# Kernel tuning notes

Hardware: AMD Instinct MI355X
Metric: run time of the kernel (lower is better)

## Reference

```python
import jax, jax.numpy as jnp
import numpy as np

B, S, D = 1, 2048, 1024
H = 16            # num_heads
DH = D // H       # head dim = 64
WIN = 128         # local window size
DIL = 4           # dilation rate


def setup_inputs() -> dict:
    key = jax.random.key(0)
    k1, k2, k3 = jax.random.split(key, 3)
    x = jax.random.normal(k1, (B, S, D), jnp.float32)
    w_qkv = jax.random.normal(k2, (D, 3 * D), jnp.float32) * 0.02
    w_out = jax.random.normal(k3, (D, D), jnp.float32) * 0.02
    return {"x": x, "w_qkv": w_qkv, "w_out": w_out}


def reference(x, w_qkv, w_out):
    b, s, d = x.shape
    scale = 1.0 / np.sqrt(DH).astype(np.float32)

    qkv = x @ w_qkv                                   # [B,S,3D]
    q, k, v = jnp.split(qkv, 3, axis=-1)
    q = q.reshape(b, s, H, DH)
    k = k.reshape(b, s, H, DH)
    v = v.reshape(b, s, H, DH)

    # ---- local window attention: attend within non-overlapping windows ----
    nw = s // WIN
    qw = q.reshape(b, nw, WIN, H, DH)
    kw = k.reshape(b, nw, WIN, H, DH)
    vw = v.reshape(b, nw, WIN, H, DH)
    s_loc = jnp.einsum('bnihd,bnjhd->bnhij', qw, kw) * scale
    p_loc = jax.nn.softmax(s_loc, axis=-1)
    o_loc = jnp.einsum('bnhij,bnjhd->bnihd', p_loc, vw).reshape(b, s, H, DH)

    # ---- dilated attention: attend within each stride-DIL residue class ----
    n = s // DIL
    # seq index = i*DIL + g  -> position i within dilation group g
    qd = q.reshape(b, n, DIL, H, DH)
    kd = k.reshape(b, n, DIL, H, DH)
    vd = v.reshape(b, n, DIL, H, DH)
    s_dil = jnp.einsum('bighd,bjghd->bghij', qd, kd) * scale
    p_dil = jax.nn.softmax(s_dil, axis=-1)
    o_dil = jnp.einsum('bghij,bjghd->bighd', p_dil, vd).reshape(b, s, H, DH)

    # ---- global full attention ----
    s_glb = jnp.einsum('bihd,bjhd->bhij', q, k) * scale
    p_glb = jax.nn.softmax(s_glb, axis=-1)
    o_glb = jnp.einsum('bhij,bjhd->bihd', p_glb, v)

    # fuse the three scales (uniform average) and project out
    o = (o_loc + o_dil + o_glb) * (1.0 / 3.0)
    return o.reshape(b, s, d) @ w_out
```

## Files before the change

### kernel.cpp

```cpp
#include <hip/hip_runtime.h>
#include <hip/hip_bf16.h>


typedef __attribute__((ext_vector_type(8))) short s8v;
typedef __attribute__((ext_vector_type(4))) float f4v;

#define QSCALE 0.18033688011112042f

__device__ __forceinline__ short f2bf(float f) {
  union { float f; unsigned u; } x; x.f = f;
  unsigned r = (x.u + 0x7FFF + ((x.u >> 16) & 1)) >> 16;
  return (short)r;
}
__device__ __forceinline__ f4v mfma16(s8v a, s8v b, f4v c) {
  return __builtin_amdgcn_mfma_f32_16x16x32_bf16(a, b, c, 0, 0, 0);
}
__device__ __forceinline__ void load_lds16(const void* g, void* l) {
  __builtin_amdgcn_global_load_lds(
      (const __attribute__((address_space(1))) unsigned int*)g,
      (__attribute__((address_space(3))) unsigned int*)l, 16, 0, 0);
}
__device__ __forceinline__ float exp2f_fast(float x) {
  return __builtin_amdgcn_exp2f(x);
}

__global__ __launch_bounds__(256)
void fill_const_kernel(float* __restrict__ out, int n, float v) {
  int i = blockIdx.x * 256 + threadIdx.x;
  if (i < n) out[i] = v;
}

__global__ __launch_bounds__(256)
void cast_f32_bf16(const float* __restrict__ src, short* __restrict__ dst, int n) {
  int i = (blockIdx.x * 256 + threadIdx.x) * 4;
  if (i < n) {
    float4 v = *reinterpret_cast<const float4*>(&src[i]);
    union { short s[4]; int2 p; } u;
    u.s[0] = f2bf(v.x); u.s[1] = f2bf(v.y); u.s[2] = f2bf(v.z); u.s[3] = f2bf(v.w);
    *reinterpret_cast<int2*>(&dst[i]) = u.p;
  }
}

__global__ __launch_bounds__(256)
void transpose_conv(const float* __restrict__ src, short* __restrict__ dst,
                    int K, int N) {
  __shared__ float T[64][69];
  const int n0 = blockIdx.x * 64, k0 = blockIdx.y * 64;
  const int t = threadIdx.x;
  for (int jb = t; jb < 1024; jb += 256) {
    int r = jb >> 4, c4 = (jb & 15) * 4;
    float4 v = *reinterpret_cast<const float4*>(&src[(size_t)(k0 + r) * N + n0 + c4]);
    T[c4 + 0][r] = v.x; T[c4 + 1][r] = v.y; T[c4 + 2][r] = v.z; T[c4 + 3][r] = v.w;
  }
  __syncthreads();
  for (int jb = t; jb < 512; jb += 256) {
    int n = jb >> 3, k8 = (jb & 7) * 8;
    union { short s[8]; int4 v; } p;
#pragma unroll
    for (int i = 0; i < 8; ++i) p.s[i] = f2bf(T[n][k8 + i]);
    *reinterpret_cast<int4*>(&dst[(size_t)(n0 + n) * K + k0 + k8]) = p.v;
  }
}

__device__ __forceinline__ void g1_epilogue_store(
    int gcol, int grow0, const f4v& a,
    short* __restrict__ qb, short* __restrict__ kb, short* __restrict__ vT) {
  if (gcol >= 2048) {
    int d = gcol - 2048;
    int j = grow0 >> 2;
    int gb = ((j >> 6) << 6) + (((j >> 5) & 1) << 5) +
             (((j >> 2) & 3) << 3) + (((j >> 4) & 1) << 2) + (j & 3);
    size_t base = (size_t)d * 2048 + gb;
#pragma unroll
    for (int r = 0; r < 4; ++r)
      vT[base + (r << 9)] = f2bf(a[r]);
  } else {
    short* dst = (gcol < 1024) ? qb : kb;
    float sc = (gcol < 1024) ? QSCALE : 1.0f;
    int c = gcol & 1023;
#pragma unroll
    for (int r = 0; r < 4; ++r)
      dst[(size_t)(grow0 + r) * 1024 + c] = f2bf(a[r] * sc);
  }
}

template <int COUT, bool AF32, int NT>
__global__ __launch_bounds__(256)
void gemm_tile(const void* __restrict__ Av, const short* __restrict__ Bt,
               short* __restrict__ qb, short* __restrict__ kb,
               short* __restrict__ vT, float* __restrict__ co,
               int K, int N) {
  __shared__ __align__(16) short As[64 * 32];
  __shared__ __align__(16) short Bs[NT * 32];
  const int tid = threadIdx.x, wave = tid >> 6;
  const int li = tid & 63;
  const int row0 = blockIdx.y * 64, col0 = blockIdx.x * NT;
  const int lr = li & 15, quad = li >> 4, lk = quad * 8;
  constexpr int NTW = NT / 64;

  f4v acc[4][NTW];
#pragma unroll
  for (int i = 0; i < 4; ++i)
#pragma unroll
    for (int j = 0; j < NTW; ++j) acc[i][j] = (f4v){0.f, 0.f, 0.f, 0.f};

  for (int k0 = 0; k0 < K; k0 += 32) {
    __syncthreads();
#pragma unroll
    for (int u = 0; u < NTW; ++u)
      load_lds16(Bt + (size_t)(col0 + u * 64 + (tid >> 2)) * K + k0 + (tid & 3) * 8,
                 &Bs[u * 2048 + wave * 512]);
    if (AF32) {
      const float* A = (const float*)Av;
#pragma unroll
      for (int c = 0; c < 2; ++c) {
        int j = c * 256 + tid;
        int r = j >> 3, c4 = (j & 7) * 4;
        float4 v = *reinterpret_cast<const float4*>(&A[(size_t)(row0 + r) * K + k0 + c4]);
        union { short s[4]; int2 v2; } p;
        p.s[0] = f2bf(v.x); p.s[1] = f2bf(v.y); p.s[2] = f2bf(v.z); p.s[3] = f2bf(v.w);
        *reinterpret_cast<int2*>(&As[r * 32 + c4]) = p.v2;
      }
    } else {
      load_lds16((const short*)Av + (size_t)(row0 + (tid >> 2)) * K + k0 + (tid & 3) * 8,
                 &As[wave * 512]);
    }
    __syncthreads();

    s8v af[4], bfr[NTW];
#pragma unroll
    for (int mt = 0; mt < 4; ++mt)
      af[mt] = *reinterpret_cast<const s8v*>(&As[(mt * 16 + lr) * 32 + lk]);
#pragma unroll
    for (int u = 0; u < NTW; ++u)
      bfr[u] = *reinterpret_cast<const s8v*>(&Bs[(wave * (NT / 4) + u * 16 + lr) * 32 + lk]);
#pragma unroll
    for (int mt = 0; mt < 4; ++mt)
#pragma unroll
      for (int u = 0; u < NTW; ++u)
        acc[mt][u] = mfma16(af[mt], bfr[u], acc[mt][u]);
  }

#pragma unroll
  for (int mt = 0; mt < 4; ++mt) {
#pragma unroll
    for (int u = 0; u < NTW; ++u) {
      int gcol = col0 + wave * (NT / 4) + u * 16 + lr;
      int grow0 = row0 + mt * 16 + quad * 4;
      if (COUT == 0) {
        g1_epilogue_store(gcol, grow0, acc[mt][u], qb, kb, vT);
      } else {
#pragma unroll
        for (int r = 0; r < 4; ++r)
          co[(size_t)(grow0 + r) * N + gcol] = acc[mt][u][r] * (1.0f / 3.0f);
      }
    }
  }
}

__global__ __launch_bounds__(512, 2)
void attn_unified(const short* __restrict__ qb, const short* __restrict__ kb,
                  const short* __restrict__ vT, short* __restrict__ o) {
  __shared__ __align__(16) short Ks[2][64][72];
  __shared__ __align__(16) short Vt[2][64][72];
  __shared__ float lX[2][4][16][4];

  const int tid = threadIdx.x;
  const int wave = tid >> 6, li = tid & 63;
  const int grp = wave >> 2, wr = wave & 3;
  const int b = blockIdx.x, h = b & 15, g = b >> 4;
  const int qcol = h * 64;
  const int lr = li & 15, quad = li >> 4, lk = quad * 8;
  const int wt2 = g >> 2;
  const int wH  = (g >> 1) & 1;
  const bool wgrp = (grp == wH);
  const int sr = tid >> 3, sc8 = (tid & 7) * 8;

  s8v q0, q1;
  {
    const short* qrow = &qb[(size_t)(g * 64 + wr * 16 + lr) * 1024 + qcol];
    q0 = *reinterpret_cast<const s8v*>(&qrow[lk]);
    q1 = *reinterpret_cast<const s8v*>(&qrow[32 + lk]);
  }

  *reinterpret_cast<int4*>(&Ks[0][sr][sc8]) =
      *reinterpret_cast<const int4*>(&kb[(size_t)(sr << 2) * 1024 + qcol + sc8]);
  *reinterpret_cast<int4*>(&Vt[0][sr][sc8]) =
      *reinterpret_cast<const int4*>(&vT[(size_t)(h * 64 + sr) * 2048 + sc8]);
  __syncthreads();

  float l_r = 0.f, l_loc = 0.f, l_dil = 0.f;
  f4v oacc[4], o_loc[4], o_dil[4];
#pragma unroll
  for (int i = 0; i < 4; ++i) {
    oacc[i]  = (f4v){0.f, 0.f, 0.f, 0.f};
    o_loc[i] = (f4v){0.f, 0.f, 0.f, 0.f};
    o_dil[i] = (f4v){0.f, 0.f, 0.f, 0.f};
  }

  const int koffA = ((grp * 2 + 0) * 16 + lr) * 72 + lk;
  const int koffB = ((grp * 2 + 1) * 16 + lr) * 72 + lk;
  const short* KsF = &Ks[0][0][0];
  const short* VtF = &Vt[0][0][0];

#pragma unroll
  for (int rho = 0; rho < 4; ++rho) {
    const float sn0 = oacc[0][rho], sn1 = oacc[1][rho],
                sn2 = oacc[2][rho], sn3 = oacc[3][rho];
    const float lsn = l_r;

#pragma unroll 2
    for (int t8 = 0; t8 < 8; ++t8) {
      const int t = rho * 8 + t8;
      const int cur = t8 & 1, nxt = cur ^ 1;
      const bool pf = (rho < 3) || (t8 < 7);
      const bool wt = wgrp && (t8 == wt2);
      const int cb = cur * 4608;

      int4 kpre, vpre;
      if (pf) {
        const int tn = t + 1;
        const int ksn = ((((tn & 7) << 6) + sr) << 2) + (tn >> 3);
        kpre = *reinterpret_cast<const int4*>(&kb[(size_t)ksn * 1024 + qcol + sc8]);
        vpre = *reinterpret_cast<const int4*>(
            &vT[(size_t)(h * 64 + sr) * 2048 + tn * 64 + sc8]);
      }

      f4v s4a = (f4v){0.f, 0.f, 0.f, 0.f};
      f4v s4b = (f4v){0.f, 0.f, 0.f, 0.f};
      s4a = mfma16(*reinterpret_cast<const s8v*>(&KsF[cb + koffA]), q0, s4a);
      s4b = mfma16(*reinterpret_cast<const s8v*>(&KsF[cb + koffB]), q0, s4b);
      s4a = mfma16(*reinterpret_cast<const s8v*>(&KsF[cb + koffA + 32]), q1, s4a);
      s4b = mfma16(*reinterpret_cast<const s8v*>(&KsF[cb + koffB + 32]), q1, s4b);

      union { short s[8]; s8v v; } pk;
      float ps = 0.f;
#pragma unroll
      for (int r = 0; r < 4; ++r) {
        float p0 = exp2f_fast(s4a[r]), p1 = exp2f_fast(s4b[r]);
        ps += p0 + p1;
        pk.s[r] = f2bf(p0); pk.s[4 + r] = f2bf(p1);
      }
      l_r += ps;
      if (wt) l_loc += ps;

      if (wt) {
#pragma unroll
        for (int nt = 0; nt < 4; ++nt) {
          s8v bv = *reinterpret_cast<const s8v*>(
              &VtF[cb + (nt * 16 + lr) * 72 + grp * 32 + lk]);
          f4v dd = mfma16(pk.v, bv, (f4v){0.f, 0.f, 0.f, 0.f});
          oacc[nt] += dd;
          o_loc[nt] += dd;
        }
      } else {
#pragma unroll
        for (int nt = 0; nt < 4; ++nt) {
          s8v bv = *reinterpret_cast<const s8v*>(
              &VtF[cb + (nt * 16 + lr) * 72 + grp * 32 + lk]);
          oacc[nt] = mfma16(pk.v, bv, oacc[nt]);
        }
      }

      if (pf) {
        *reinterpret_cast<int4*>(&Ks[nxt][sr][sc8]) = kpre;
        *reinterpret_cast<int4*>(&Vt[nxt][sr][sc8]) = vpre;
      }
      __syncthreads();
    }

    if (((lr ^ rho) & 3) == 0) l_dil = l_r - lsn;
    o_dil[0][rho] = oacc[0][rho] - sn0;
    o_dil[1][rho] = oacc[1][rho] - sn1;
    o_dil[2][rho] = oacc[2][rho] - sn2;
    o_dil[3][rho] = oacc[3][rho] - sn3;
  }

  l_r   += __shfl_xor(l_r, 16);   l_r   += __shfl_xor(l_r, 32);
  l_loc += __shfl_xor(l_loc, 16); l_loc += __shfl_xor(l_loc, 32);
  l_dil += __shfl_xor(l_dil, 16); l_dil += __shfl_xor(l_dil, 32);
  if (li < 16) {
    lX[grp][wr][li][0] = l_r;
    lX[grp][wr][li][1] = l_loc;
    lX[grp][wr][li][2] = l_dil;
  }
  __syncthreads();

  f4v part[4];
#pragma unroll
  for (int r = 0; r < 4; ++r) {
    int q4 = quad * 4 + r;
    float lg = lX[0][wr][q4][0] + lX[1][wr][q4][0];
    float ll = lX[0][wr][q4][1] + lX[1][wr][q4][1];
    float ld = lX[0][wr][q4][2] + lX[1][wr][q4][2];
    float ig = 1.0f / lg, il = 1.0f / ll, id = 1.0f / ld;
#pragma unroll
    for (int nt = 0; nt < 4; ++nt)
      part[nt][r] = oacc[nt][r] * ig + o_loc[nt][r] * il + o_dil[nt][r] * id;
  }

  float* xch = reinterpret_cast<float*>(&Ks[0][0][0]);
  const int slot = wr * 64 + li;
  if (grp == 1) {
#pragma unroll
    for (int nt = 0; nt < 4; ++nt)
#pragma unroll
      for (int hh = 0; hh < 2; ++hh) {
        float2 v2 = make_float2(part[nt][2 * hh], part[nt][2 * hh + 1]);
        *reinterpret_cast<float2*>(&xch[slot * 18 + (nt * 2 + hh) * 2]) = v2;
      }
  }
  __syncthreads();
  if (grp == 0) {
#pragma unroll
    for (int nt = 0; nt < 4; ++nt)
#pragma unroll
      for (int hh = 0; hh < 2; ++hh) {
        float2 v2 = *reinterpret_cast<const float2*>(&xch[slot * 18 + (nt * 2 + hh) * 2]);
        part[nt][2 * hh]     += v2.x;
        part[nt][2 * hh + 1] += v2.y;
      }
#pragma unroll
    for (int r = 0; r < 4; ++r) {
      int qs = g * 64 + wr * 16 + quad * 4 + r;
#pragma unroll
      for (int nt = 0; nt < 4; ++nt)
        o[(size_t)qs * 1024 + qcol + nt * 16 + lr] = f2bf(part[nt][r]);
    }
  }
}

extern "C" void kernel_launch(void* const* d_in, const int* in_sizes, int n_in,
                              void* d_out, int out_size, void* d_ws, size_t ws_size,
                              hipStream_t stream) {
  float* out = (float*)d_out;
  const int nfill = (out_size + 255) / 256;
  if (n_in != 3) { fill_const_kernel<<<nfill, 256, 0, stream>>>(out, out_size, 0.5f); return; }
  int ix = -1, iq = -1, io = -1;
  for (int i = 0; i < 3; ++i) {
    if      (in_sizes[i] == 2097152) ix = i;
    else if (in_sizes[i] == 3145728) iq = i;
    else if (in_sizes[i] == 1048576) io = i;
  }
  if (ix < 0 || iq < 0 || io < 0) { fill_const_kernel<<<nfill, 256, 0, stream>>>(out, out_size, 0.3f); return; }
  const float* x     = (const float*)d_in[ix];
  const float* w_qkv = (const float*)d_in[iq];
  const float* w_out = (const float*)d_in[io];

  char* ws = (char*)d_ws;
  const size_t MB = 1048576;
  const size_t needX = 22 * MB;
  const size_t needY = 20 * MB;

  if (ws_size >= needX) {
    short* qb     = (short*)(ws);
    short* kb     = (short*)(ws + 4 * MB);
    short* vT     = (short*)(ws + 8 * MB);
    short* w_qkvT = (short*)(ws + 12 * MB);
    short* xb     = (short*)(ws + 18 * MB);
    short* o      = (short*)(ws + 12 * MB);
    short* w_outT = (short*)(ws + 16 * MB);
    cast_f32_bf16<<<2048, 256, 0, stream>>>(x, xb, 2097152);
    transpose_conv<<<dim3(48, 16), 256, 0, stream>>>(w_qkv, w_qkvT, 1024, 3072);
    gemm_tile<0, false, 192><<<dim3(16, 32), 256, 0, stream>>>(xb, w_qkvT, qb, kb, vT, nullptr, 1024, 3072);
    transpose_conv<<<dim3(16, 16), 256, 0, stream>>>(w_out, w_outT, 1024, 1024);
    attn_unified<<<512, 512, 0, stream>>>(qb, kb, vT, o);
    gemm_tile<1, false, 64><<<dim3(16, 32), 256, 0, stream>>>(o, w_outT, nullptr, nullptr, nullptr, out, 1024, 1024);
  } else if (ws_size >= needY) {
    short* w_outT = (short*)(ws);
    short* qb     = (short*)(ws + 2 * MB);
    short* kb     = (short*)(ws + 6 * MB);
    short* vT     = (short*)(ws + 10 * MB);
    short* w_qkvT = (short*)(ws + 14 * MB);
    short* o      = (short*)(ws + 14 * MB);
    transpose_conv<<<dim3(48, 16), 256, 0, stream>>>(w_qkv, w_qkvT, 1024, 3072);
    transpose_conv<<<dim3(16, 16), 256, 0, stream>>>(w_out, w_outT, 1024, 1024);
    gemm_tile<0, true, 192><<<dim3(16, 32), 256, 0, stream>>>(x, w_qkvT, qb, kb, vT, nullptr, 1024, 3072);
    attn_unified<<<512, 512, 0, stream>>>(qb, kb, vT, o);
    gemm_tile<1, false, 64><<<dim3(16, 32), 256, 0, stream>>>(o, w_outT, nullptr, nullptr, nullptr, out, 1024, 1024);
  } else {
    fill_const_kernel<<<nfill, 256, 0, stream>>>(out, out_size, 0.2f);
  }
}
```

Measured before the change: 167.0 us.

## Fuse prep kernels into one launch, widen GEMM K-step, retile QKV GEMM

The separate x cast and the two weight transpose kernels are merged into one prep_fused launch, using a block-index split to pick the task. This removes launch overhead and serialization between small kernels. The GEMM now stages two 32-wide K slices per barrier pair, so it syncs half as often at the cost of doubled LDS. The QKV GEMM tile width drops from 192 to 128 columns, giving more blocks, and the workspace layout is enlarged to 24 MB, which may force the fallback path on smaller workspaces.

After: 149.8 us. -10.3%, faster.

```diff
diff --git a/kernel.cpp b/kernel.cpp
--- a/kernel.cpp
+++ b/kernel.cpp
@@ -31,22 +31,27 @@
 }
 
 __global__ __launch_bounds__(256)
-void cast_f32_bf16(const float* __restrict__ src, short* __restrict__ dst, int n) {
-  int i = (blockIdx.x * 256 + threadIdx.x) * 4;
-  if (i < n) {
-    float4 v = *reinterpret_cast<const float4*>(&src[i]);
-    union { short s[4]; int2 p; } u;
-    u.s[0] = f2bf(v.x); u.s[1] = f2bf(v.y); u.s[2] = f2bf(v.z); u.s[3] = f2bf(v.w);
-    *reinterpret_cast<int2*>(&dst[i]) = u.p;
-  }
-}
-
-__global__ __launch_bounds__(256)
-void transpose_conv(const float* __restrict__ src, short* __restrict__ dst,
-                    int K, int N) {
+void prep_fused(const float* __restrict__ wq, short* __restrict__ wqT,
+                const float* __restrict__ wo, short* __restrict__ woT,
+                const float* __restrict__ x, short* __restrict__ xb) {
+  const int bx = blockIdx.x, t = threadIdx.x;
   __shared__ float T[64][69];
-  const int n0 = blockIdx.x * 64, k0 = blockIdx.y * 64;
-  const int t = threadIdx.x;
+  if (bx >= 64) {
+    if (x) {
+      int cb = (bx - 64) * 16 + blockIdx.y;
+      int i = (cb * 256 + t) * 4;
+      float4 v = *reinterpret_cast<const float4*>(&x[i]);
+      union { short s[4]; int2 p; } u;
+      u.s[0] = f2bf(v.x); u.s[1] = f2bf(v.y); u.s[2] = f2bf(v.z); u.s[3] = f2bf(v.w);
+      *reinterpret_cast<int2*>(&xb[i]) = u.p;
+    }
+    return;
+  }
+  const float* src; short* dst; int N, bxx;
+  if (bx < 48) { src = wq; dst = wqT; N = 3072; bxx = bx; }
+  else         { src = wo; dst = woT; N = 1024; bxx = bx - 48; }
+  const int K = 1024;
+  const int n0 = bxx * 64, k0 = blockIdx.y * 64;
   for (int jb = t; jb < 1024; jb += 256) {
     int r = jb >> 4, c4 = (jb & 15) * 4;
     float4 v = *reinterpret_cast<const float4*>(&src[(size_t)(k0 + r) * N + n0 + c4]);
@@ -90,8 +95,8 @@
                short* __restrict__ qb, short* __restrict__ kb,
                short* __restrict__ vT, float* __restrict__ co,
                int K, int N) {
-  __shared__ __align__(16) short As[64 * 32];
-  __shared__ __align__(16) short Bs[NT * 32];
+  __shared__ __align__(16) short As[2][64 * 32];
+  __shared__ __align__(16) short Bs[2][NT * 32];
   const int tid = threadIdx.x, wave = tid >> 6;
   const int li = tid & 63;
   const int row0 = blockIdx.y * 64, col0 = blockIdx.x * NT;
@@ -104,41 +109,48 @@
 #pragma unroll
     for (int j = 0; j < NTW; ++j) acc[i][j] = (f4v){0.f, 0.f, 0.f, 0.f};
 
-  for (int k0 = 0; k0 < K; k0 += 32) {
+  for (int k0 = 0; k0 < K; k0 += 64) {
     __syncthreads();
 #pragma unroll
-    for (int u = 0; u < NTW; ++u)
-      load_lds16(Bt + (size_t)(col0 + u * 64 + (tid >> 2)) * K + k0 + (tid & 3) * 8,
-                 &Bs[u * 2048 + wave * 512]);
-    if (AF32) {
-      const float* A = (const float*)Av;
-#pragma unroll
-      for (int c = 0; c < 2; ++c) {
-        int j = c * 256 + tid;
-        int r = j >> 3, c4 = (j & 7) * 4;
-        float4 v = *reinterpret_cast<const float4*>(&A[(size_t)(row0 + r) * K + k0 + c4]);
-        union { short s[4]; int2 v2; } p;
-        p.s[0] = f2bf(v.x); p.s[1] = f2bf(v.y); p.s[2] = f2bf(v.z); p.s[3] = f2bf(v.w);
-        *reinterpret_cast<int2*>(&As[r * 32 + c4]) = p.v2;
-      }
-    } else {
-      load_lds16((const short*)Av + (size_t)(row0 + (tid >> 2)) * K + k0 + (tid & 3) * 8,
-                 &As[wave * 512]);
+    for (int kk = 0; kk < 2; ++kk) {
+#pragma unroll
+      for (int u = 0; u < NTW; ++u)
+        load_lds16(Bt + (size_t)(col0 + u * 64 + (tid >> 2)) * K + k0 + kk * 32 + (tid & 3) * 8,
+                   &Bs[kk][u * 2048 + wave * 512]);
+      if (AF32) {
+        const float* A = (const float*)Av;
+#pragma unroll
+        for (int c = 0; c < 2; ++c) {
+          int j = c * 256 + tid;
+          int r = j >> 3, c4 = (j & 7) * 4;
+          float4 v = *reinterpret_cast<const float4*>(
+              &A[(size_t)(row0 + r) * K + k0 + kk * 32 + c4]);
+          union { short s[4]; int2 v2; } p;
+          p.s[0] = f2bf(v.x); p.s[1] = f2bf(v.y); p.s[2] = f2bf(v.z); p.s[3] = f2bf(v.w);
+          *reinterpret_cast<int2*>(&As[kk][r * 32 + c4]) = p.v2;
+        }
+      } else {
+        load_lds16((const short*)Av + (size_t)(row0 + (tid >> 2)) * K + k0 + kk * 32 + (tid & 3) * 8,
+                   &As[kk][wave * 512]);
+      }
     }
     __syncthreads();
 
-    s8v af[4], bfr[NTW];
-#pragma unroll
-    for (int mt = 0; mt < 4; ++mt)
-      af[mt] = *reinterpret_cast<const s8v*>(&As[(mt * 16 + lr) * 32 + lk]);
-#pragma unroll
-    for (int u = 0; u < NTW; ++u)
-      bfr[u] = *reinterpret_cast<const s8v*>(&Bs[(wave * (NT / 4) + u * 16 + lr) * 32 + lk]);
-#pragma unroll
-    for (int mt = 0; mt < 4; ++mt)
+#pragma unroll
+    for (int kk = 0; kk < 2; ++kk) {
+      s8v af[4], bfr[NTW];
+#pragma unroll
+      for (int mt = 0; mt < 4; ++mt)
+        af[mt] = *reinterpret_cast<const s8v*>(&As[kk][(mt * 16 + lr) * 32 + lk]);
 #pragma unroll
       for (int u = 0; u < NTW; ++u)
-        acc[mt][u] = mfma16(af[mt], bfr[u], acc[mt][u]);
+        bfr[u] = *reinterpret_cast<const s8v*>(&Bs[kk][(wave * (NT / 4) + u * 16 + lr) * 32 + lk]);
+#pragma unroll
+      for (int mt = 0; mt < 4; ++mt)
+#pragma unroll
+        for (int u = 0; u < NTW; ++u)
+          acc[mt][u] = mfma16(af[mt], bfr[u], acc[mt][u]);
+    }
   }
 
 #pragma unroll
@@ -349,7 +361,7 @@
 
   char* ws = (char*)d_ws;
   const size_t MB = 1048576;
-  const size_t needX = 22 * MB;
+  const size_t needX = 24 * MB;
   const size_t needY = 20 * MB;
 
   if (ws_size >= needX) {
@@ -357,13 +369,11 @@
     short* kb     = (short*)(ws + 4 * MB);
     short* vT     = (short*)(ws + 8 * MB);
     short* w_qkvT = (short*)(ws + 12 * MB);
-    short* xb     = (short*)(ws + 18 * MB);
     short* o      = (short*)(ws + 12 * MB);
-    short* w_outT = (short*)(ws + 16 * MB);
-    cast_f32_bf16<<<2048, 256, 0, stream>>>(x, xb, 2097152);
-    transpose_conv<<<dim3(48, 16), 256, 0, stream>>>(w_qkv, w_qkvT, 1024, 3072);
-    gemm_tile<0, false, 192><<<dim3(16, 32), 256, 0, stream>>>(xb, w_qkvT, qb, kb, vT, nullptr, 1024, 3072);
-    transpose_conv<<<dim3(16, 16), 256, 0, stream>>>(w_out, w_outT, 1024, 1024);
+    short* w_outT = (short*)(ws + 18 * MB);
+    short* xb     = (short*)(ws + 20 * MB);
+    prep_fused<<<dim3(192, 16), 256, 0, stream>>>(w_qkv, w_qkvT, w_out, w_outT, x, xb);
+    gemm_tile<0, false, 128><<<dim3(24, 32), 256, 0, stream>>>(xb, w_qkvT, qb, kb, vT, nullptr, 1024, 3072);
     attn_unified<<<512, 512, 0, stream>>>(qb, kb, vT, o);
     gemm_tile<1, false, 64><<<dim3(16, 32), 256, 0, stream>>>(o, w_outT, nullptr, nullptr, nullptr, out, 1024, 1024);
   } else if (ws_size >= needY) {
@@ -373,9 +383,8 @@
     short* vT     = (short*)(ws + 10 * MB);
     short* w_qkvT = (short*)(ws + 14 * MB);
     short* o      = (short*)(ws + 14 * MB);
-    transpose_conv<<<dim3(48, 16), 256, 0, stream>>>(w_qkv, w_qkvT, 1024, 3072);
-    transpose_conv<<<dim3(16, 16), 256, 0, stream>>>(w_out, w_outT, 1024, 1024);
-    gemm_tile<0, true, 192><<<dim3(16, 32), 256, 0, stream>>>(x, w_qkvT, qb, kb, vT, nullptr, 1024, 3072);
+    prep_fused<<<dim3(64, 16), 256, 0, stream>>>(w_qkv, w_qkvT, w_out, w_outT, nullptr, nullptr);
+    gemm_tile<0, true, 128><<<dim3(24, 32), 256, 0, stream>>>(x, w_qkvT, qb, kb, vT, nullptr, 1024, 3072);
     attn_unified<<<512, 512, 0, stream>>>(qb, kb, vT, o);
     gemm_tile<1, false, 64><<<dim3(16, 32), 256, 0, stream>>>(o, w_outT, nullptr, nullptr, nullptr, out, 1024, 1024);
   } else {
```
